# Kernel tuning notes

Measured on AMD Instinct MI355X. Metric: run time of the kernel, lower is better.

Reference implementation:

```python
import jax, jax.numpy as jnp
import numpy as np

N_NODES = 100_000
N_EDGES = 1_600_000
N_FEAT = 64
E_FEAT = 32
OUT_FEAT = 64


def _xavier_normal(key, shape, gain):
    fan_out, fan_in = shape
    std = gain * np.sqrt(2.0 / (fan_in + fan_out))
    return jax.random.normal(key, shape, dtype=jnp.float32) * std


def setup_inputs() -> dict:
    key = jax.random.key(0)
    ks = jax.random.split(key, 9)
    d_cat = 2 * N_FEAT + E_FEAT  # 160
    n_feat = jax.random.normal(ks[0], (N_NODES, N_FEAT), dtype=jnp.float32)
    e_feat = jax.random.normal(ks[1], (N_EDGES, E_FEAT), dtype=jnp.float32)
    src = jax.random.randint(ks[2], (N_EDGES,), 0, N_NODES, dtype=jnp.int32)
    dst = jax.random.randint(ks[3], (N_EDGES,), 0, N_NODES, dtype=jnp.int32)
    gain = np.sqrt(2.0)
    bound_msg = 1.0 / np.sqrt(d_cat)
    return {
        "n_feat": n_feat,
        "e_feat": e_feat,
        "src": src,
        "dst": dst,
        # W_msg uses default torch Linear init (kaiming-uniform-ish); exact init irrelevant for correctness
        "W_msg_w": jax.random.uniform(ks[4], (OUT_FEAT, d_cat), jnp.float32, -bound_msg, bound_msg),
        "W_msg_b": jax.random.uniform(ks[5], (OUT_FEAT,), jnp.float32, -bound_msg, bound_msg),
        # W uses xavier_normal with gain sqrt(2)
        "W_w": _xavier_normal(ks[6], (2 * OUT_FEAT, d_cat), gain),
        "W_b": jax.random.uniform(ks[7], (2 * OUT_FEAT,), jnp.float32, -bound_msg, bound_msg),
        "a": _xavier_normal(ks[8], (2 * OUT_FEAT, 1), gain),
    }


def reference(n_feat, e_feat, src, dst, W_msg_w, W_msg_b, W_w, W_b, a):
    # gather: per-edge concat [E, 2*n_feat + e_feat]
    feat_cat = jnp.concatenate([n_feat[src], n_feat[dst], e_feat], axis=1)
    # edge attention logits: leaky_relu((feat_cat @ W^T + b) @ a)  -> [E]
    w_feat = feat_cat @ W_w.T + W_b                      # [E, 2*out_feat]
    logits = jax.nn.leaky_relu(w_feat @ a[:, 0])         # [E]
    # edge softmax grouped by destination node
    seg_max = jax.ops.segment_max(logits, dst, num_segments=N_NODES)  # [N]
    ex = jnp.exp(logits - seg_max[dst])                  # [E]
    seg_sum = jax.ops.segment_sum(ex, dst, num_segments=N_NODES)     # [N]
    att = ex / seg_sum[dst]                              # [E]
    # messages and weighted scatter-sum aggregation
    msg = feat_cat @ W_msg_w.T + W_msg_b                 # [E, out_feat]
    agg = jax.ops.segment_sum(att[:, None] * msg, dst, num_segments=N_NODES)  # [N, out_feat]
    return jax.nn.relu(agg)
```

## Files before the change

### kernel.cpp

```cpp
#include <hip/hip_runtime.h>
#include <hip/hip_bf16.h>

#define N_NODES 100000
#define N_EDGES 1600000
#define NF 64
#define EF 32

#define SCAN_B 512
#define SCAN_NB ((N_NODES + SCAN_B - 1) / SCAN_B)


__global__ __launch_bounds__(256) void k0_prep(
    const float* __restrict__ Ww, const float* __restrict__ Wb,
    const float* __restrict__ a, const float* __restrict__ Wmsg,
    float* __restrict__ v, float* __restrict__ W1T, float* __restrict__ W2T,
    float* __restrict__ WmeT) {
  int t = threadIdx.x;
  for (int j = t; j < 160; j += 256) {
    float s = 0.f;
    for (int k = 0; k < 128; ++k) s = fmaf(a[k], Ww[k * 160 + j], s);
    v[j] = s;
  }
  if (t == 0) {
    float s = 0.f;
    for (int k = 0; k < 128; ++k) s = fmaf(a[k], Wb[k], s);
    v[160] = s;
  }
  for (int idx = t; idx < 64 * 64; idx += 256) {
    int j = idx >> 6, i = idx & 63;
    W1T[idx] = Wmsg[i * 160 + j];
    W2T[idx] = Wmsg[i * 160 + 64 + j];
  }
  for (int idx = t; idx < 32 * 64; idx += 256) {
    int j = idx >> 6, i = idx & 63;
    WmeT[idx] = Wmsg[i * 160 + 128 + j];
  }
}

__global__ __launch_bounds__(256) void k1_node(
    const float* __restrict__ nf_g, const float* __restrict__ v,
    const float* __restrict__ W1T, const float* __restrict__ W2T,
    float* __restrict__ s1, float* __restrict__ s2,
    float* __restrict__ m_src, float* __restrict__ m_dst) {
  int n = blockIdx.x * 256 + threadIdx.x;
  if (n >= N_NODES) return;
  const float4* nf4 = (const float4*)(nf_g + (size_t)n * NF);
  float acc[64];
#pragma unroll
  for (int i = 0; i < 64; ++i) acc[i] = 0.f;
  float s1a = 0.f, s2a = 0.f;
  for (int j4 = 0; j4 < 16; ++j4) {
    float4 q = nf4[j4];
    float xs[4] = {q.x, q.y, q.z, q.w};
#pragma unroll
    for (int u = 0; u < 4; ++u) {
      int j = j4 * 4 + u;
      float x = xs[u];
      s1a = fmaf(v[j], x, s1a);
      s2a = fmaf(v[64 + j], x, s2a);
      const float* w = W1T + j * 64;
#pragma unroll
      for (int i = 0; i < 64; ++i) acc[i] = fmaf(w[i], x, acc[i]);
    }
  }
  s1[n] = s1a;
  s2[n] = s2a;
  float* ms = m_src + (size_t)n * NF;
#pragma unroll
  for (int i = 0; i < 64; ++i) ms[i] = acc[i];
#pragma unroll
  for (int i = 0; i < 64; ++i) acc[i] = 0.f;
  for (int j4 = 0; j4 < 16; ++j4) {
    float4 q = nf4[j4];
    float xs[4] = {q.x, q.y, q.z, q.w};
#pragma unroll
    for (int u = 0; u < 4; ++u) {
      int j = j4 * 4 + u;
      float x = xs[u];
      const float* w = W2T + j * 64;
#pragma unroll
      for (int i = 0; i < 64; ++i) acc[i] = fmaf(w[i], x, acc[i]);
    }
  }
  float* md = m_dst + (size_t)n * NF;
#pragma unroll
  for (int i = 0; i < 64; ++i) md[i] = acc[i];
}

__global__ __launch_bounds__(256) void k_count(const int* __restrict__ dst,
                                               int* __restrict__ cnt) {
  int e = blockIdx.x * 256 + threadIdx.x;
  if (e < N_EDGES) atomicAdd(&cnt[dst[e]], 1);
}

__global__ __launch_bounds__(SCAN_B) void kS1(const int* __restrict__ cnt,
                                              int* __restrict__ bsum) {
  __shared__ int sh[SCAN_B];
  int t = threadIdx.x;
  int i = blockIdx.x * SCAN_B + t;
  sh[t] = (i < N_NODES) ? cnt[i] : 0;
  __syncthreads();
  for (int d = SCAN_B / 2; d > 0; d >>= 1) {
    if (t < d) sh[t] += sh[t + d];
    __syncthreads();
  }
  if (t == 0) bsum[blockIdx.x] = sh[0];
}

__global__ __launch_bounds__(256) void kS2(const int* __restrict__ bsum,
                                           int* __restrict__ boff,
                                           int* __restrict__ row_ptr) {
  __shared__ int sh[256];
  int t = threadIdx.x;
  sh[t] = (t < SCAN_NB) ? bsum[t] : 0;
  __syncthreads();
  for (int d = 1; d < 256; d <<= 1) {
    int val = (t >= d) ? sh[t - d] : 0;
    __syncthreads();
    sh[t] += val;
    __syncthreads();
  }
  if (t < SCAN_NB) boff[t] = (t == 0) ? 0 : sh[t - 1];
  if (t == 255) row_ptr[N_NODES] = sh[255];
}

__global__ __launch_bounds__(SCAN_B) void kS3(const int* __restrict__ cnt,
                                              const int* __restrict__ boff,
                                              int* __restrict__ row_ptr,
                                              int* __restrict__ cursor) {
  __shared__ int sh[SCAN_B];
  int t = threadIdx.x;
  int i = blockIdx.x * SCAN_B + t;
  int val = (i < N_NODES) ? cnt[i] : 0;
  sh[t] = val;
  __syncthreads();
  for (int d = 1; d < SCAN_B; d <<= 1) {
    int u = (t >= d) ? sh[t - d] : 0;
    __syncthreads();
    sh[t] += u;
    __syncthreads();
  }
  if (i < N_NODES) {
    int excl = boff[blockIdx.x] + sh[t] - val;
    row_ptr[i] = excl;
    cursor[i] = excl;
  }
}

__global__ __launch_bounds__(256) void kE_scatter(
    const int* __restrict__ src, const int* __restrict__ dst,
    const float* __restrict__ e_feat, const float* __restrict__ s1,
    const float* __restrict__ s2, const float* __restrict__ v,
    int* __restrict__ cursor, unsigned long long* __restrict__ edata) {
  int e = blockIdx.x * 256 + threadIdx.x;
  if (e >= N_EDGES) return;
  int sn = src[e], dn = dst[e];
  const float4* efr = (const float4*)(e_feat + (size_t)e * EF);
  float t = 0.f;
#pragma unroll
  for (int i = 0; i < 8; ++i) {
    float4 q = efr[i];
    t = fmaf(q.x, v[128 + i * 4 + 0], t);
    t = fmaf(q.y, v[128 + i * 4 + 1], t);
    t = fmaf(q.z, v[128 + i * 4 + 2], t);
    t = fmaf(q.w, v[128 + i * 4 + 3], t);
  }
  float lg = s1[sn] + s2[dn] + t + v[160];
  float l = lg > 0.f ? lg : 0.01f * lg;
  float ex = __expf(l);
  int p = atomicAdd(&cursor[dn], 1);
  unsigned long long pk = ((unsigned long long)(unsigned)e << 43) |
                          ((unsigned long long)(unsigned)sn << 26) |
                          (unsigned long long)(__float_as_uint(ex) >> 6);
  edata[p] = pk;
}

__global__ __launch_bounds__(256) void k3_agg(
    const int* __restrict__ row_ptr, const int2* __restrict__ edata,
    const float* __restrict__ e_feat, const float* __restrict__ m_src,
    const float* __restrict__ m_dst, const float* __restrict__ WmeT,
    const float* __restrict__ Wmsg_b, float* __restrict__ out) {
  int lane = threadIdx.x & 63;
  int wid = threadIdx.x >> 6;
  int n = blockIdx.x * 4 + wid;
  if (n >= N_NODES) return;
  int start = row_ptr[n];
  int end = row_ptr[n + 1];
  int half = lane >> 5;
  int col = lane & 31;
  float sum_ex = 0.f, acc_ms = 0.f, acc_ef = 0.f;
  for (int base = start; base < end; base += 64) {
    int2 md = make_int2(0, 0);
    if (base + lane < end) md = edata[base + lane];
    int m = end - base;
    if (m > 64) m = 64;
    int mm4 = (m + 3) & ~3;
    for (int k = 0; k < mm4; k += 4) {
      int ek[4], sk[4];
      float exk[4], msk[4], efh[2], exh[2];
#pragma unroll
      for (int u = 0; u < 4; ++u) {
        unsigned lo = (unsigned)__shfl(md.x, k + u);
        unsigned hi = (unsigned)__shfl(md.y, k + u);
        ek[u] = (int)(hi >> 11);
        sk[u] = (int)(((hi & 0x7FFu) << 6) | (lo >> 26));
        exk[u] = __uint_as_float((lo & 0x3FFFFFFu) << 6);
      }
      int eh0 = half ? ek[1] : ek[0];
      int eh1 = half ? ek[3] : ek[2];
      exh[0] = half ? exk[1] : exk[0];
      exh[1] = half ? exk[3] : exk[2];
#pragma unroll
      for (int u = 0; u < 4; ++u)
        msk[u] = m_src[(size_t)sk[u] * NF + lane];
      efh[0] = e_feat[(size_t)eh0 * EF + col];
      efh[1] = e_feat[(size_t)eh1 * EF + col];
#pragma unroll
      for (int u = 0; u < 4; ++u) {
        sum_ex += exk[u];
        acc_ms = fmaf(exk[u], msk[u], acc_ms);
      }
      acc_ef = fmaf(exh[0], efh[0], acc_ef);
      acc_ef = fmaf(exh[1], efh[1], acc_ef);
    }
  }
  float mm = 0.f;
#pragma unroll
  for (int j = 0; j < 32; ++j) {
    float efj = __shfl(acc_ef, j) + __shfl(acc_ef, j + 32);
    mm = fmaf(WmeT[j * 64 + lane], efj, mm);
  }
  float o = 0.f;
  if (sum_ex > 0.f) {
    o = (acc_ms + mm) / sum_ex + m_dst[(size_t)n * NF + lane] + Wmsg_b[lane];
    o = fmaxf(o, 0.f);
  }
  out[(size_t)n * NF + lane] = o;
}

extern "C" void kernel_launch(void* const* d_in, const int* in_sizes, int n_in,
                              void* d_out, int out_size, void* d_ws,
                              size_t ws_size, hipStream_t stream) {
  const float* n_feat = (const float*)d_in[0];
  const float* e_feat = (const float*)d_in[1];
  const int* src = (const int*)d_in[2];
  const int* dst = (const int*)d_in[3];
  const float* Wmsg_w = (const float*)d_in[4];
  const float* Wmsg_b = (const float*)d_in[5];
  const float* W_w = (const float*)d_in[6];
  const float* W_b = (const float*)d_in[7];
  const float* a = (const float*)d_in[8];
  float* out = (float*)d_out;

  char* ws = (char*)d_ws;
  size_t off = 0;
  auto alloc = [&](size_t bytes) -> char* {
    char* p = ws + off;
    off = (off + bytes + 255) & ~(size_t)255;
    return p;
  };
  float* v = (float*)alloc(161 * 4);
  float* W1T = (float*)alloc(64 * 64 * 4);
  float* W2T = (float*)alloc(64 * 64 * 4);
  float* WmeT = (float*)alloc(32 * 64 * 4);
  float* s1 = (float*)alloc(N_NODES * 4);
  float* s2 = (float*)alloc(N_NODES * 4);
  float* m_src = (float*)alloc((size_t)N_NODES * NF * 4);
  float* m_dst = (float*)alloc((size_t)N_NODES * NF * 4);
  int* cnt = (int*)alloc(N_NODES * 4);
  int* row_ptr = (int*)alloc((N_NODES + 1) * 4);
  int* cursor = (int*)alloc(N_NODES * 4);
  int* bsum = (int*)alloc(SCAN_NB * 4);
  int* boff = (int*)alloc(SCAN_NB * 4);
  unsigned long long* edata = (unsigned long long*)alloc((size_t)N_EDGES * 8);
  if (off > ws_size) return;

  k0_prep<<<1, 256, 0, stream>>>(W_w, W_b, a, Wmsg_w, v, W1T, W2T, WmeT);
  k1_node<<<(N_NODES + 255) / 256, 256, 0, stream>>>(n_feat, v, W1T, W2T, s1,
                                                     s2, m_src, m_dst);
  hipMemsetAsync(cnt, 0, N_NODES * 4, stream);
  k_count<<<(N_EDGES + 255) / 256, 256, 0, stream>>>(dst, cnt);
  kS1<<<SCAN_NB, SCAN_B, 0, stream>>>(cnt, bsum);
  kS2<<<1, 256, 0, stream>>>(bsum, boff, row_ptr);
  kS3<<<SCAN_NB, SCAN_B, 0, stream>>>(cnt, boff, row_ptr, cursor);
  kE_scatter<<<(N_EDGES + 255) / 256, 256, 0, stream>>>(src, dst, e_feat, s1,
                                                        s2, v, cursor, edata);
  k3_agg<<<(N_NODES + 3) / 4, 256, 0, stream>>>(row_ptr, (const int2*)edata,
                                                e_feat, m_src, m_dst, WmeT,
                                                Wmsg_b, out);
}
```

Measured before the change: 627.7 us.

## Store node messages in bf16 and move edge-feature logit into aggregation

Node message tables m_src/m_dst are stored as bf16, halving their footprint and the bytes of the random gathers in the aggregation kernel. The edge-feature dot product for the attention logit is removed from the scatter kernel and recomputed in the aggregation kernel from the e_feat row it already loads, using a cross-lane reduction, so e_feat is read once instead of twice. The count kernel reads dst as int4, and the aggregation loop processes 8 edges per step. The cost is bf16 rounding error in messages and extra shuffles and exp work inside the aggregation loop.

```diff
diff --git a/kernel.cpp b/kernel.cpp
--- a/kernel.cpp
+++ b/kernel.cpp
@@ -9,6 +9,11 @@
 #define SCAN_B 512
 #define SCAN_NB ((N_NODES + SCAN_B - 1) / SCAN_B)
 
+
+__device__ __forceinline__ unsigned f2bf_rn(float x) {
+  unsigned u = __float_as_uint(x);
+  return (u + 0x7FFFu + ((u >> 16) & 1u)) >> 16;
+}
 
 __global__ __launch_bounds__(256) void k0_prep(
     const float* __restrict__ Ww, const float* __restrict__ Wb,
@@ -41,7 +46,7 @@
     const float* __restrict__ nf_g, const float* __restrict__ v,
     const float* __restrict__ W1T, const float* __restrict__ W2T,
     float* __restrict__ s1, float* __restrict__ s2,
-    float* __restrict__ m_src, float* __restrict__ m_dst) {
+    unsigned* __restrict__ m_srcH, unsigned* __restrict__ m_dstH) {
   int n = blockIdx.x * 256 + threadIdx.x;
   if (n >= N_NODES) return;
   const float4* nf4 = (const float4*)(nf_g + (size_t)n * NF);
@@ -65,9 +70,10 @@
   }
   s1[n] = s1a;
   s2[n] = s2a;
-  float* ms = m_src + (size_t)n * NF;
-#pragma unroll
-  for (int i = 0; i < 64; ++i) ms[i] = acc[i];
+  unsigned* ms = m_srcH + (size_t)n * 32;
+#pragma unroll
+  for (int i = 0; i < 32; ++i)
+    ms[i] = f2bf_rn(acc[2 * i]) | (f2bf_rn(acc[2 * i + 1]) << 16);
 #pragma unroll
   for (int i = 0; i < 64; ++i) acc[i] = 0.f;
   for (int j4 = 0; j4 < 16; ++j4) {
@@ -82,15 +88,22 @@
       for (int i = 0; i < 64; ++i) acc[i] = fmaf(w[i], x, acc[i]);
     }
   }
-  float* md = m_dst + (size_t)n * NF;
-#pragma unroll
-  for (int i = 0; i < 64; ++i) md[i] = acc[i];
-}
-
-__global__ __launch_bounds__(256) void k_count(const int* __restrict__ dst,
+  unsigned* md = m_dstH + (size_t)n * 32;
+#pragma unroll
+  for (int i = 0; i < 32; ++i)
+    md[i] = f2bf_rn(acc[2 * i]) | (f2bf_rn(acc[2 * i + 1]) << 16);
+}
+
+__global__ __launch_bounds__(256) void k_count(const int4* __restrict__ dst4,
                                                int* __restrict__ cnt) {
-  int e = blockIdx.x * 256 + threadIdx.x;
-  if (e < N_EDGES) atomicAdd(&cnt[dst[e]], 1);
+  int i = blockIdx.x * 256 + threadIdx.x;
+  if (i < N_EDGES / 4) {
+    int4 d = dst4[i];
+    atomicAdd(&cnt[d.x], 1);
+    atomicAdd(&cnt[d.y], 1);
+    atomicAdd(&cnt[d.z], 1);
+    atomicAdd(&cnt[d.w], 1);
+  }
 }
 
 __global__ __launch_bounds__(SCAN_B) void kS1(const int* __restrict__ cnt,
@@ -149,37 +162,26 @@
 
 __global__ __launch_bounds__(256) void kE_scatter(
     const int* __restrict__ src, const int* __restrict__ dst,
-    const float* __restrict__ e_feat, const float* __restrict__ s1,
-    const float* __restrict__ s2, const float* __restrict__ v,
-    int* __restrict__ cursor, unsigned long long* __restrict__ edata) {
+    const float* __restrict__ s1, const float* __restrict__ s2,
+    const float* __restrict__ v, int* __restrict__ cursor,
+    unsigned long long* __restrict__ edata) {
   int e = blockIdx.x * 256 + threadIdx.x;
   if (e >= N_EDGES) return;
   int sn = src[e], dn = dst[e];
-  const float4* efr = (const float4*)(e_feat + (size_t)e * EF);
-  float t = 0.f;
-#pragma unroll
-  for (int i = 0; i < 8; ++i) {
-    float4 q = efr[i];
-    t = fmaf(q.x, v[128 + i * 4 + 0], t);
-    t = fmaf(q.y, v[128 + i * 4 + 1], t);
-    t = fmaf(q.z, v[128 + i * 4 + 2], t);
-    t = fmaf(q.w, v[128 + i * 4 + 3], t);
-  }
-  float lg = s1[sn] + s2[dn] + t + v[160];
-  float l = lg > 0.f ? lg : 0.01f * lg;
-  float ex = __expf(l);
+  float bb = s1[sn] + s2[dn] + v[160];
   int p = atomicAdd(&cursor[dn], 1);
   unsigned long long pk = ((unsigned long long)(unsigned)e << 43) |
                           ((unsigned long long)(unsigned)sn << 26) |
-                          (unsigned long long)(__float_as_uint(ex) >> 6);
+                          (unsigned long long)(__float_as_uint(bb) >> 6);
   edata[p] = pk;
 }
 
 __global__ __launch_bounds__(256) void k3_agg(
     const int* __restrict__ row_ptr, const int2* __restrict__ edata,
-    const float* __restrict__ e_feat, const float* __restrict__ m_src,
-    const float* __restrict__ m_dst, const float* __restrict__ WmeT,
-    const float* __restrict__ Wmsg_b, float* __restrict__ out) {
+    const float* __restrict__ e_feat, const unsigned short* __restrict__ m_srcH,
+    const unsigned short* __restrict__ m_dstH, const float* __restrict__ v,
+    const float* __restrict__ WmeT, const float* __restrict__ Wmsg_b,
+    float* __restrict__ out) {
   int lane = threadIdx.x & 63;
   int wid = threadIdx.x >> 6;
   int n = blockIdx.x * 4 + wid;
@@ -188,40 +190,60 @@
   int end = row_ptr[n + 1];
   int half = lane >> 5;
   int col = lane & 31;
+  float v3 = v[128 + col];
   float sum_ex = 0.f, acc_ms = 0.f, acc_ef = 0.f;
-  for (int base = start; base < end; base += 64) {
-    int2 md = make_int2(0, 0);
-    if (base + lane < end) md = edata[base + lane];
-    int m = end - base;
+  for (int cb = start; cb < end; cb += 64) {
+    int2 md = make_int2(0x03FE0000, 0);
+    if (cb + lane < end) md = edata[cb + lane];
+    int m = end - cb;
     if (m > 64) m = 64;
-    int mm4 = (m + 3) & ~3;
-    for (int k = 0; k < mm4; k += 4) {
-      int ek[4], sk[4];
-      float exk[4], msk[4], efh[2], exh[2];
-#pragma unroll
-      for (int u = 0; u < 4; ++u) {
+    int mm8 = (m + 7) & ~7;
+    for (int k = 0; k < mm8; k += 8) {
+      int ek[8], sk[8];
+      float bs[8];
+#pragma unroll
+      for (int u = 0; u < 8; ++u) {
         unsigned lo = (unsigned)__shfl(md.x, k + u);
         unsigned hi = (unsigned)__shfl(md.y, k + u);
         ek[u] = (int)(hi >> 11);
         sk[u] = (int)(((hi & 0x7FFu) << 6) | (lo >> 26));
-        exk[u] = __uint_as_float((lo & 0x3FFFFFFu) << 6);
+        bs[u] = __uint_as_float((lo & 0x3FFFFFFu) << 6);
       }
-      int eh0 = half ? ek[1] : ek[0];
-      int eh1 = half ? ek[3] : ek[2];
-      exh[0] = half ? exk[1] : exk[0];
-      exh[1] = half ? exk[3] : exk[2];
-#pragma unroll
-      for (int u = 0; u < 4; ++u)
-        msk[u] = m_src[(size_t)sk[u] * NF + lane];
-      efh[0] = e_feat[(size_t)eh0 * EF + col];
-      efh[1] = e_feat[(size_t)eh1 * EF + col];
-#pragma unroll
-      for (int u = 0; u < 4; ++u) {
-        sum_ex += exk[u];
-        acc_ms = fmaf(exk[u], msk[u], acc_ms);
+      unsigned short msr[8];
+#pragma unroll
+      for (int u = 0; u < 8; ++u)
+        msr[u] = m_srcH[(size_t)sk[u] * NF + lane];
+      float efh[4];
+#pragma unroll
+      for (int p = 0; p < 4; ++p) {
+        int ep = half ? ek[2 * p + 1] : ek[2 * p];
+        efh[p] = e_feat[(size_t)ep * EF + col];
       }
-      acc_ef = fmaf(exh[0], efh[0], acc_ef);
-      acc_ef = fmaf(exh[1], efh[1], acc_ef);
+      float exq[4];
+#pragma unroll
+      for (int p = 0; p < 4; ++p) {
+        float t = efh[p] * v3;
+        t += __shfl_xor(t, 1);
+        t += __shfl_xor(t, 2);
+        t += __shfl_xor(t, 4);
+        t += __shfl_xor(t, 8);
+        t += __shfl_xor(t, 16);
+        float bb = half ? bs[2 * p + 1] : bs[2 * p];
+        float lg = bb + t;
+        float l = lg > 0.f ? lg : 0.01f * lg;
+        exq[p] = __expf(l);
+        acc_ef = fmaf(exq[p], efh[p], acc_ef);
+      }
+#pragma unroll
+      for (int p = 0; p < 4; ++p) {
+        float ex0 = __shfl(exq[p], 0);
+        float ex1 = __shfl(exq[p], 32);
+        sum_ex += ex0 + ex1;
+        float ms0 = __uint_as_float((unsigned)msr[2 * p] << 16);
+        float ms1 = __uint_as_float((unsigned)msr[2 * p + 1] << 16);
+        acc_ms = fmaf(ex0, ms0, acc_ms);
+        acc_ms = fmaf(ex1, ms1, acc_ms);
+      }
     }
   }
   float mm = 0.f;
@@ -232,7 +254,9 @@
   }
   float o = 0.f;
   if (sum_ex > 0.f) {
-    o = (acc_ms + mm) / sum_ex + m_dst[(size_t)n * NF + lane] + Wmsg_b[lane];
+    float mdv =
+        __uint_as_float((unsigned)m_dstH[(size_t)n * NF + lane] << 16);
+    o = (acc_ms + mm) / sum_ex + mdv + Wmsg_b[lane];
     o = fmaxf(o, 0.f);
   }
   out[(size_t)n * NF + lane] = o;
@@ -265,8 +289,8 @@
   float* WmeT = (float*)alloc(32 * 64 * 4);
   float* s1 = (float*)alloc(N_NODES * 4);
   float* s2 = (float*)alloc(N_NODES * 4);
-  float* m_src = (float*)alloc((size_t)N_NODES * NF * 4);
-  float* m_dst = (float*)alloc((size_t)N_NODES * NF * 4);
+  unsigned* m_srcH = (unsigned*)alloc((size_t)N_NODES * NF * 2);
+  unsigned* m_dstH = (unsigned*)alloc((size_t)N_NODES * NF * 2);
   int* cnt = (int*)alloc(N_NODES * 4);
   int* row_ptr = (int*)alloc((N_NODES + 1) * 4);
   int* cursor = (int*)alloc(N_NODES * 4);
@@ -277,15 +301,16 @@
 
   k0_prep<<<1, 256, 0, stream>>>(W_w, W_b, a, Wmsg_w, v, W1T, W2T, WmeT);
   k1_node<<<(N_NODES + 255) / 256, 256, 0, stream>>>(n_feat, v, W1T, W2T, s1,
-                                                     s2, m_src, m_dst);
+                                                     s2, m_srcH, m_dstH);
   hipMemsetAsync(cnt, 0, N_NODES * 4, stream);
-  k_count<<<(N_EDGES + 255) / 256, 256, 0, stream>>>(dst, cnt);
+  k_count<<<(N_EDGES / 4 + 255) / 256, 256, 0, stream>>>((const int4*)dst,
+                                                         cnt);
   kS1<<<SCAN_NB, SCAN_B, 0, stream>>>(cnt, bsum);
   kS2<<<1, 256, 0, stream>>>(bsum, boff, row_ptr);
   kS3<<<SCAN_NB, SCAN_B, 0, stream>>>(cnt, boff, row_ptr, cursor);
-  kE_scatter<<<(N_EDGES + 255) / 256, 256, 0, stream>>>(src, dst, e_feat, s1,
-                                                        s2, v, cursor, edata);
-  k3_agg<<<(N_NODES + 3) / 4, 256, 0, stream>>>(row_ptr, (const int2*)edata,
-                                                e_feat, m_src, m_dst, WmeT,
-                                                Wmsg_b, out);
-}
+  kE_scatter<<<(N_EDGES + 255) / 256, 256, 0, stream>>>(src, dst, s1, s2, v,
+                                                        cursor, edata);
+  k3_agg<<<(N_NODES + 3) / 4, 256, 0, stream>>>(
+      row_ptr, (const int2*)edata, e_feat, (const unsigned short*)m_srcH,
+      (const unsigned short*)m_dstH, v, WmeT, Wmsg_b, out);
+}
```

After: 746.0 us. 1.19x slower.
